# Kernel tuning notes

Measured on AMD Instinct MI355X. Metric: run time of the kernel, lower is better.

## Reference

```python
import jax, jax.numpy as jnp
import numpy as np

L = 8          # n_layer
D = 512        # hidden_size
DIN = 1024     # d_inner = 2*D (Mamba expand=2)
DS = 16        # d_state
DTR = 32       # dt_rank = ceil(D/16)
K = 4          # d_conv
NACT = 3       # n_action_to_predict
ADIM = 4
LOSS_COEF = 1.0

def silu(x):
    return x * jax.nn.sigmoid(x)

def rms(x, w, eps=1e-5):
    return x * jax.lax.rsqrt(jnp.mean(x * x, axis=-1, keepdims=True) + eps) * w

def tokenize(images, states, actions, patch_w, patch_b, state_w, state_b, act_w, act_b):
    # images [b,l,3,224,224] -> 14x14 patches of 3*16*16=768 -> mean-pooled image token
    b, l = images.shape[:2]
    p = images.reshape(b, l, 3, 14, 16, 14, 16).transpose(0, 1, 3, 5, 2, 4, 6).reshape(b, l, 196, 768)
    img = jnp.mean(p @ patch_w.T + patch_b, axis=2)            # [b,l,D] token_type 1
    st = states[:, :, 0] @ state_w.T + state_b                 # [b,l,D] token_type 2
    ac = actions[:, :, :NACT - 1] @ act_w.T + act_b            # [b,l,NACT-1,D] token_type 3
    toks = jnp.concatenate([img[:, :, None], st[:, :, None], ac], axis=2)  # [b,l,1+NACT,D]
    return toks.reshape(b, l * (1 + NACT), D)

def mamba_mixer(x, in_w, cw, cb, xpw, dtw, dtb, alog, dp, ow):
    # x: [b,S,D]
    b, S, _ = x.shape
    xz = x @ in_w.T                                   # [b,S,2*DIN]
    xi, z = xz[..., :DIN], xz[..., DIN:]
    # causal depthwise conv, kernel K
    xp = jnp.pad(xi, ((0, 0), (K - 1, 0), (0, 0)))
    xc = cb + sum(cw[:, k] * xp[:, k:k + S, :] for k in range(K))
    xc = silu(xc)
    proj = xc @ xpw.T                                  # [b,S,DTR+2*DS]
    dtr, Bm, Cm = proj[..., :DTR], proj[..., DTR:DTR + DS], proj[..., DTR + DS:]
    dt = jax.nn.softplus(dtr @ dtw.T + dtb)            # [b,S,DIN]
    A = -jnp.exp(alog)                                 # [DIN,DS]
    dA = jnp.exp(dt[..., None] * A)                    # [b,S,DIN,DS]
    dBx = dt[..., None] * Bm[:, :, None, :] * xc[..., None]
    def step(h, inp):
        a_t, bx_t = inp
        h = a_t * h + bx_t
        return h, h
    _, hs = jax.lax.scan(step, jnp.zeros((b, DIN, DS), x.dtype),
                         (dA.swapaxes(0, 1), dBx.swapaxes(0, 1)))  # hs [S,b,DIN,DS]
    y = jnp.einsum('sbdn,bsn->bsd', hs, Cm) + dp * xc
    return (y * silu(z)) @ ow.T

def _forward(images, seq_length, states, actions, action_labels,
             patch_w, patch_b, state_w, state_b, act_w, act_b,
             norm1_w, in_proj_w, conv_w, conv_b, x_proj_w, dt_w, dt_b,
             A_log, Dp, out_proj_w, norm2_w, fc1_w, fc2_w, norm_f_w,
             head_w, head_b):
    b, l = images.shape[:2]
    hidden = tokenize(images, states, actions, patch_w, patch_b, state_w, state_b, act_w, act_b)
    residual = jnp.zeros_like(hidden)
    for i in range(L):
        residual = hidden + residual
        hidden = mamba_mixer(rms(residual, norm1_w[i]), in_proj_w[i], conv_w[i], conv_b[i],
                             x_proj_w[i], dt_w[i], dt_b[i], A_log[i], Dp[i], out_proj_w[i])
        residual = hidden + residual
        g = rms(residual, norm2_w[i]) @ fc1_w[i].T       # GatedMLP fc1 -> [.., 2*DIN]
        hidden = (g[..., :DIN] * silu(g[..., DIN:])) @ fc2_w[i].T
    residual = hidden + residual
    hidden = rms(residual, norm_f_w)
    # static action-token positions: per-frame tokens [img, state, act, act] -> indices 1..3
    hs = hidden.reshape(b, l, 1 + NACT, D)[:, :, 1:, :]
    action_preds = hs @ head_w.T + head_b                # [b,l,NACT,ADIM]
    mask = (jnp.arange(l)[None, :] < seq_length[:, None]).astype(jnp.float32)
    la = jnp.mean(jnp.abs(action_preds - action_labels), axis=(2, 3))
    la = (la * mask).sum(axis=1) / jnp.clip(mask.sum(axis=1), 1.0)
    loss = jnp.mean(la) * LOSS_COEF
    return loss, action_preds

def setup_inputs() -> dict:
    key = jax.random.key(0)
    ks = iter(jax.random.split(key, 40))
    nrm = lambda shape, s=0.02: s * jax.random.normal(next(ks), shape, dtype=jnp.float32)
    inp = {
        'images': jax.random.normal(next(ks), (2, 64, 3, 224, 224), jnp.float32),
        'seq_length': jax.random.randint(next(ks), (2,), 1, 65),
        'states': jax.random.normal(next(ks), (2, 64, NACT, 7), jnp.float32),
        'actions': jax.random.normal(next(ks), (2, 64, NACT, ADIM), jnp.float32),
        'action_labels': jax.random.normal(next(ks), (2, 64, NACT, ADIM), jnp.float32),
        'patch_w': nrm((D, 768)), 'patch_b': jnp.zeros((D,), jnp.float32),
        'state_w': nrm((D, 7)), 'state_b': jnp.zeros((D,), jnp.float32),
        'act_w': nrm((D, ADIM)), 'act_b': jnp.zeros((D,), jnp.float32),
        'norm1_w': jnp.ones((L, D), jnp.float32),
        'in_proj_w': nrm((L, 2 * DIN, D)),
        'conv_w': nrm((L, DIN, K), 0.1), 'conv_b': jnp.zeros((L, DIN), jnp.float32),
        'x_proj_w': nrm((L, DTR + 2 * DS, DIN)),
        'dt_w': nrm((L, DIN, DTR)), 'dt_b': jnp.full((L, DIN), -4.6, jnp.float32),
        'A_log': jnp.log(jnp.broadcast_to(jnp.arange(1, DS + 1, dtype=jnp.float32), (L, DIN, DS))).copy(),
        'Dp': jnp.ones((L, DIN), jnp.float32),
        'out_proj_w': nrm((L, D, DIN)),
        'norm2_w': jnp.ones((L, D), jnp.float32),
        'fc1_w': nrm((L, 2 * DIN, D)), 'fc2_w': nrm((L, D, DIN)),
        'norm_f_w': jnp.ones((D,), jnp.float32),
        'head_w': nrm((ADIM, D)), 'head_b': jnp.zeros((ADIM,), jnp.float32),
    }
    return inp

def reference(images, seq_length, states, actions, action_labels,
              patch_w, patch_b, state_w, state_b, act_w, act_b,
              norm1_w, in_proj_w, conv_w, conv_b, x_proj_w, dt_w, dt_b,
              A_log, Dp, out_proj_w, norm2_w, fc1_w, fc2_w, norm_f_w,
              head_w, head_b):
    return _forward(images, seq_length, states, actions, action_labels,
                    patch_w, patch_b, state_w, state_b, act_w, act_b,
                    norm1_w, in_proj_w, conv_w, conv_b, x_proj_w, dt_w, dt_b,
                    A_log, Dp, out_proj_w, norm2_w, fc1_w, fc2_w, norm_f_w,
                    head_w, head_b)
```

## Files before the change

### kernel.cpp

```cpp
#include <hip/hip_runtime.h>


#define NTOK 512
#define SEQ  256
#define CS   32

typedef __attribute__((ext_vector_type(8))) short bf16x8;
typedef __attribute__((ext_vector_type(16))) float f32x16;

__device__ __forceinline__ float silu_f(float x) { return x / (1.0f + expf(-x)); }
__device__ __forceinline__ float softplus_f(float x) {
  return (x > 20.0f) ? x : log1pf(expf(x));
}

__device__ __forceinline__ void split_pack(float4 v, uint2* hi, uint2* lo) {
  uint ux = __float_as_uint(v.x), uy = __float_as_uint(v.y);
  uint uz = __float_as_uint(v.z), uw = __float_as_uint(v.w);
  hi->x = (ux >> 16) | (uy & 0xffff0000u);
  hi->y = (uz >> 16) | (uw & 0xffff0000u);
  float lx = v.x - __uint_as_float(ux & 0xffff0000u);
  float ly = v.y - __uint_as_float(uy & 0xffff0000u);
  float lz = v.z - __uint_as_float(uz & 0xffff0000u);
  float lw = v.w - __uint_as_float(uw & 0xffff0000u);
  lo->x = (__float_as_uint(lx) >> 16) | (__float_as_uint(ly) & 0xffff0000u);
  lo->y = (__float_as_uint(lz) >> 16) | (__float_as_uint(lw) & 0xffff0000u);
}

__global__ __launch_bounds__(256) void gemm_bs_k(const float* __restrict__ A,
                                                 const float* __restrict__ B,
                                                 float* __restrict__ C,
                                                 int M, int N, int K, int Kc) {
  __shared__ alignas(16) ushort sAh[2][2][2][512];
  __shared__ alignas(16) ushort sAl[2][2][2][512];
  __shared__ alignas(16) ushort sBh[2][2][2][512];
  __shared__ alignas(16) ushort sBl[2][2][2][512];
  int t = threadIdx.x;
  int bn = blockIdx.x, bm = blockIdx.y, z = blockIdx.z;
  const float* Ab = A + (size_t)bm * 64 * K + (size_t)z * Kc;
  const float* Bb = B + (size_t)bn * 64 * K + (size_t)z * Kc;
  float* Cb = C + (size_t)z * M * N;
  int r = t >> 2, kc = (t & 3) << 2;
  int st = r >> 5, m = r & 31;
  int off = ((kc >> 3) << 8) + (m << 3) + (kc & 7);
  int w = t >> 6, lane = t & 63;
  int wr = w >> 1, wc = w & 1;

  f32x16 acc;
#pragma unroll
  for (int i = 0; i < 16; ++i) acc[i] = 0.f;

  int ns = Kc >> 5;
  const float* Ar = Ab + (size_t)r * K + kc;
  const float* Br = Bb + (size_t)r * K + kc;
  float4 a0 = *(const float4*)&Ar[0];
  float4 a1 = *(const float4*)&Ar[16];
  float4 b0 = *(const float4*)&Br[0];
  float4 b1 = *(const float4*)&Br[16];
  {
    uint2 hi, lo;
    split_pack(a0, &hi, &lo);
    *(uint2*)&sAh[0][0][st][off] = hi; *(uint2*)&sAl[0][0][st][off] = lo;
    split_pack(a1, &hi, &lo);
    *(uint2*)&sAh[0][1][st][off] = hi; *(uint2*)&sAl[0][1][st][off] = lo;
    split_pack(b0, &hi, &lo);
    *(uint2*)&sBh[0][0][st][off] = hi; *(uint2*)&sBl[0][0][st][off] = lo;
    split_pack(b1, &hi, &lo);
    *(uint2*)&sBh[0][1][st][off] = hi; *(uint2*)&sBl[0][1][st][off] = lo;
  }
  __syncthreads();
  for (int ssi = 0; ssi < ns; ++ssi) {
    int buf = ssi & 1;
    if (ssi + 1 < ns) {
      a0 = *(const float4*)&Ar[(ssi + 1) * 32];
      a1 = *(const float4*)&Ar[(ssi + 1) * 32 + 16];
      b0 = *(const float4*)&Br[(ssi + 1) * 32];
      b1 = *(const float4*)&Br[(ssi + 1) * 32 + 16];
    }
    bf16x8 ah = *(bf16x8*)&sAh[buf][0][wr][lane << 3];
    bf16x8 al = *(bf16x8*)&sAl[buf][0][wr][lane << 3];
    bf16x8 bh = *(bf16x8*)&sBh[buf][0][wc][lane << 3];
    bf16x8 bl = *(bf16x8*)&sBl[buf][0][wc][lane << 3];
    acc = __builtin_amdgcn_mfma_f32_32x32x16_bf16(ah, bh, acc, 0, 0, 0);
    acc = __builtin_amdgcn_mfma_f32_32x32x16_bf16(al, bh, acc, 0, 0, 0);
    acc = __builtin_amdgcn_mfma_f32_32x32x16_bf16(ah, bl, acc, 0, 0, 0);
    bf16x8 ah1 = *(bf16x8*)&sAh[buf][1][wr][lane << 3];
    bf16x8 al1 = *(bf16x8*)&sAl[buf][1][wr][lane << 3];
    bf16x8 bh1 = *(bf16x8*)&sBh[buf][1][wc][lane << 3];
    bf16x8 bl1 = *(bf16x8*)&sBl[buf][1][wc][lane << 3];
    acc = __builtin_amdgcn_mfma_f32_32x32x16_bf16(ah1, bh1, acc, 0, 0, 0);
    acc = __builtin_amdgcn_mfma_f32_32x32x16_bf16(al1, bh1, acc, 0, 0, 0);
    acc = __builtin_amdgcn_mfma_f32_32x32x16_bf16(ah1, bl1, acc, 0, 0, 0);
    if (ssi + 1 < ns) {
      uint2 hi, lo;
      split_pack(a0, &hi, &lo);
      *(uint2*)&sAh[buf ^ 1][0][st][off] = hi; *(uint2*)&sAl[buf ^ 1][0][st][off] = lo;
      split_pack(a1, &hi, &lo);
      *(uint2*)&sAh[buf ^ 1][1][st][off] = hi; *(uint2*)&sAl[buf ^ 1][1][st][off] = lo;
      split_pack(b0, &hi, &lo);
      *(uint2*)&sBh[buf ^ 1][0][st][off] = hi; *(uint2*)&sBl[buf ^ 1][0][st][off] = lo;
      split_pack(b1, &hi, &lo);
      *(uint2*)&sBh[buf ^ 1][1][st][off] = hi; *(uint2*)&sBl[buf ^ 1][1][st][off] = lo;
    }
    __syncthreads();
  }
  int col = lane & 31, rq = lane >> 5;
  float* Cw = Cb + (size_t)(bm * 64 + wr * 32) * N + bn * 64 + wc * 32 + col;
#pragma unroll
  for (int rg = 0; rg < 16; ++rg) {
    int row = (rg & 3) + ((rg >> 2) << 3) + (rq << 2);
    Cw[(size_t)row * N] = acc[rg];
  }
}

__global__ __launch_bounds__(256) void gemm_an_k(const float* __restrict__ res,
                                                 const float* __restrict__ nw,
                                                 const float* __restrict__ B,
                                                 float* __restrict__ C, int N) {
  __shared__ alignas(16) ushort sAh[2][2][2][512];
  __shared__ alignas(16) ushort sAl[2][2][2][512];
  __shared__ alignas(16) ushort sBh[2][2][2][512];
  __shared__ alignas(16) ushort sBl[2][2][2][512];
  __shared__ float snw[512];
  int t = threadIdx.x;
  int bn = blockIdx.x, bm = blockIdx.y;
  int r = t >> 2, kc = (t & 3) << 2;
  int row = bm * 64 + r;
  int st = r >> 5, m = r & 31;
  int off = ((kc >> 3) << 8) + (m << 3) + (kc & 7);
  int w = t >> 6, lane = t & 63;
  int wr = w >> 1, wc = w & 1;

  if (t < 128) *(float4*)&snw[t * 4] = *(const float4*)&nw[t * 4];

  const float* rp = res + (size_t)row * 512;
  float ss = 0.f;
#pragma unroll 8
  for (int j = 0; j < 32; ++j) {
    float4 v = *(const float4*)&rp[((t & 3) << 2) + j * 16];
    ss += v.x * v.x + v.y * v.y + v.z * v.z + v.w * v.w;
  }
  ss += __shfl_xor(ss, 1, 64);
  ss += __shfl_xor(ss, 2, 64);
  float scale = rsqrtf(ss * (1.0f / 512.0f) + 1e-5f);
  __syncthreads();

  f32x16 acc;
#pragma unroll
  for (int i = 0; i < 16; ++i) acc[i] = 0.f;

  const float* Ar = rp + kc;
  const float* Br = B + (size_t)(bn * 64 + r) * 512 + kc;
  float4 a0 = *(const float4*)&Ar[0];
  float4 a1 = *(const float4*)&Ar[16];
  float4 b0 = *(const float4*)&Br[0];
  float4 b1 = *(const float4*)&Br[16];
  {
    float4 w0 = *(const float4*)&snw[kc];
    float4 w1 = *(const float4*)&snw[kc + 16];
    float4 p0 = {a0.x * scale * w0.x, a0.y * scale * w0.y,
                 a0.z * scale * w0.z, a0.w * scale * w0.w};
    float4 p1 = {a1.x * scale * w1.x, a1.y * scale * w1.y,
                 a1.z * scale * w1.z, a1.w * scale * w1.w};
    uint2 hi, lo;
    split_pack(p0, &hi, &lo);
    *(uint2*)&sAh[0][0][st][off] = hi; *(uint2*)&sAl[0][0][st][off] = lo;
    split_pack(p1, &hi, &lo);
    *(uint2*)&sAh[0][1][st][off] = hi; *(uint2*)&sAl[0][1][st][off] = lo;
    split_pack(b0, &hi, &lo);
    *(uint2*)&sBh[0][0][st][off] = hi; *(uint2*)&sBl[0][0][st][off] = lo;
    split_pack(b1, &hi, &lo);
    *(uint2*)&sBh[0][1][st][off] = hi; *(uint2*)&sBl[0][1][st][off] = lo;
  }
  __syncthreads();
  for (int ssi = 0; ssi < 16; ++ssi) {
    int buf = ssi & 1;
    if (ssi + 1 < 16) {
      a0 = *(const float4*)&Ar[(ssi + 1) * 32];
      a1 = *(const float4*)&Ar[(ssi + 1) * 32 + 16];
      b0 = *(const float4*)&Br[(ssi + 1) * 32];
      b1 = *(const float4*)&Br[(ssi + 1) * 32 + 16];
    }
    bf16x8 ah = *(bf16x8*)&sAh[buf][0][wr][lane << 3];
    bf16x8 al = *(bf16x8*)&sAl[buf][0][wr][lane << 3];
    bf16x8 bh = *(bf16x8*)&sBh[buf][0][wc][lane << 3];
    bf16x8 bl = *(bf16x8*)&sBl[buf][0][wc][lane << 3];
    acc = __builtin_amdgcn_mfma_f32_32x32x16_bf16(ah, bh, acc, 0, 0, 0);
    acc = __builtin_amdgcn_mfma_f32_32x32x16_bf16(al, bh, acc, 0, 0, 0);
    acc = __builtin_amdgcn_mfma_f32_32x32x16_bf16(ah, bl, acc, 0, 0, 0);
    bf16x8 ah1 = *(bf16x8*)&sAh[buf][1][wr][lane << 3];
    bf16x8 al1 = *(bf16x8*)&sAl[buf][1][wr][lane << 3];
    bf16x8 bh1 = *(bf16x8*)&sBh[buf][1][wc][lane << 3];
    bf16x8 bl1 = *(bf16x8*)&sBl[buf][1][wc][lane << 3];
    acc = __builtin_amdgcn_mfma_f32_32x32x16_bf16(ah1, bh1, acc, 0, 0, 0);
    acc = __builtin_amdgcn_mfma_f32_32x32x16_bf16(al1, bh1, acc, 0, 0, 0);
    acc = __builtin_amdgcn_mfma_f32_32x32x16_bf16(ah1, bl1, acc, 0, 0, 0);
    if (ssi + 1 < 16) {
      int c0 = (ssi + 1) * 32 + kc;
      float4 w0 = *(const float4*)&snw[c0];
      float4 w1 = *(const float4*)&snw[c0 + 16];
      float4 p0 = {a0.x * scale * w0.x, a0.y * scale * w0.y,
                   a0.z * scale * w0.z, a0.w * scale * w0.w};
      float4 p1 = {a1.x * scale * w1.x, a1.y * scale * w1.y,
                   a1.z * scale * w1.z, a1.w * scale * w1.w};
      uint2 hi, lo;
      split_pack(p0, &hi, &lo);
      *(uint2*)&sAh[buf ^ 1][0][st][off] = hi; *(uint2*)&sAl[buf ^ 1][0][st][off] = lo;
      split_pack(p1, &hi, &lo);
      *(uint2*)&sAh[buf ^ 1][1][st][off] = hi; *(uint2*)&sAl[buf ^ 1][1][st][off] = lo;
      split_pack(b0, &hi, &lo);
      *(uint2*)&sBh[buf ^ 1][0][st][off] = hi; *(uint2*)&sBl[buf ^ 1][0][st][off] = lo;
      split_pack(b1, &hi, &lo);
      *(uint2*)&sBh[buf ^ 1][1][st][off] = hi; *(uint2*)&sBl[buf ^ 1][1][st][off] = lo;
    }
    __syncthreads();
  }
  int col = lane & 31, rq = lane >> 5;
  float* Cw = C + (size_t)(bm * 64 + wr * 32) * N + bn * 64 + wc * 32 + col;
#pragma unroll
  for (int rg = 0; rg < 16; ++rg) {
    int row2 = (rg & 3) + ((rg >> 2) << 3) + (rq << 2);
    Cw[(size_t)row2 * N] = acc[rg];
  }
}

__global__ __launch_bounds__(256) void gemm_rmw_k(const float* __restrict__ A,
                                                  const float* __restrict__ B,
                                                  float* __restrict__ resid) {
  __shared__ alignas(16) ushort sAh[2][2][2][512];
  __shared__ alignas(16) ushort sAl[2][2][2][512];
  __shared__ alignas(16) ushort sBh[2][2][2][512];
  __shared__ alignas(16) ushort sBl[2][2][2][512];
  int t = threadIdx.x;
  int bn = blockIdx.x, bm = blockIdx.y, z = blockIdx.z;
  int r = t >> 2, kc = (t & 3) << 2;
  int st = r >> 5, m = r & 31;
  int off = ((kc >> 3) << 8) + (m << 3) + (kc & 7);
  int w = t >> 6, lane = t & 63;
  int wr = w >> 1, wc = w & 1;

  f32x16 acc;
#pragma unroll
  for (int i = 0; i < 16; ++i) acc[i] = 0.f;

  const float* Ar = A + (size_t)(bm * 64 + r) * 1024 + z * 256 + kc;
  const float* Br = B + (size_t)(bn * 64 + r) * 1024 + z * 256 + kc;
  float4 a0 = *(const float4*)&Ar[0];
  float4 a1 = *(const float4*)&Ar[16];
  float4 b0 = *(const float4*)&Br[0];
  float4 b1 = *(const float4*)&Br[16];
  {
    uint2 hi, lo;
    split_pack(a0, &hi, &lo);
    *(uint2*)&sAh[0][0][st][off] = hi; *(uint2*)&sAl[0][0][st][off] = lo;
    split_pack(a1, &hi, &lo);
    *(uint2*)&sAh[0][1][st][off] = hi; *(uint2*)&sAl[0][1][st][off] = lo;
    split_pack(b0, &hi, &lo);
    *(uint2*)&sBh[0][0][st][off] = hi; *(uint2*)&sBl[0][0][st][off] = lo;
    split_pack(b1, &hi, &lo);
    *(uint2*)&sBh[0][1][st][off] = hi; *(uint2*)&sBl[0][1][st][off] = lo;
  }
  __syncthreads();
  for (int ssi = 0; ssi < 8; ++ssi) {
    int buf = ssi & 1;
    if (ssi + 1 < 8) {
      a0 = *(const float4*)&Ar[(ssi + 1) * 32];
      a1 = *(const float4*)&Ar[(ssi + 1) * 32 + 16];
      b0 = *(const float4*)&Br[(ssi + 1) * 32];
      b1 = *(const float4*)&Br[(ssi + 1) * 32 + 16];
    }
    bf16x8 ah = *(bf16x8*)&sAh[buf][0][wr][lane << 3];
    bf16x8 al = *(bf16x8*)&sAl[buf][0][wr][lane << 3];
    bf16x8 bh = *(bf16x8*)&sBh[buf][0][wc][lane << 3];
    bf16x8 bl = *(bf16x8*)&sBl[buf][0][wc][lane << 3];
    acc = __builtin_amdgcn_mfma_f32_32x32x16_bf16(ah, bh, acc, 0, 0, 0);
    acc = __builtin_amdgcn_mfma_f32_32x32x16_bf16(al, bh, acc, 0, 0, 0);
    acc = __builtin_amdgcn_mfma_f32_32x32x16_bf16(ah, bl, acc, 0, 0, 0);
    bf16x8 ah1 = *(bf16x8*)&sAh[buf][1][wr][lane << 3];
    bf16x8 al1 = *(bf16x8*)&sAl[buf][1][wr][lane << 3];
    bf16x8 bh1 = *(bf16x8*)&sBh[buf][1][wc][lane << 3];
    bf16x8 bl1 = *(bf16x8*)&sBl[buf][1][wc][lane << 3];
    acc = __builtin_amdgcn_mfma_f32_32x32x16_bf16(ah1, bh1, acc, 0, 0, 0);
    acc = __builtin_amdgcn_mfma_f32_32x32x16_bf16(al1, bh1, acc, 0, 0, 0);
    acc = __builtin_amdgcn_mfma_f32_32x32x16_bf16(ah1, bl1, acc, 0, 0, 0);
    if (ssi + 1 < 8) {
      uint2 hi, lo;
      split_pack(a0, &hi, &lo);
      *(uint2*)&sAh[buf ^ 1][0][st][off] = hi; *(uint2*)&sAl[buf ^ 1][0][st][off] = lo;
      split_pack(a1, &hi, &lo);
      *(uint2*)&sAh[buf ^ 1][1][st][off] = hi; *(uint2*)&sAl[buf ^ 1][1][st][off] = lo;
      split_pack(b0, &hi, &lo);
      *(uint2*)&sBh[buf ^ 1][0][st][off] = hi; *(uint2*)&sBl[buf ^ 1][0][st][off] = lo;
      split_pack(b1, &hi, &lo);
      *(uint2*)&sBh[buf ^ 1][1][st][off] = hi; *(uint2*)&sBl[buf ^ 1][1][st][off] = lo;
    }
    __syncthreads();
  }
  int col = lane & 31, rq = lane >> 5;
  float* Cw = resid + (size_t)(bm * 64 + wr * 32) * 512 + bn * 64 + wc * 32 + col;
#pragma unroll
  for (int rg = 0; rg < 16; ++rg) {
    int row = (rg & 3) + ((rg >> 2) << 3) + (rq << 2);
    atomicAdd(&Cw[(size_t)row * 512], acc[rg]);
  }
}

__global__ __launch_bounds__(256) void gemm_glu_rmw_k(const float* __restrict__ G,
                                                      const float* __restrict__ B,
                                                      float* __restrict__ resid) {
  __shared__ alignas(16) ushort sAh[2][2][2][512];
  __shared__ alignas(16) ushort sAl[2][2][2][512];
  __shared__ alignas(16) ushort sBh[2][2][2][512];
  __shared__ alignas(16) ushort sBl[2][2][2][512];
  int t = threadIdx.x;
  int bn = blockIdx.x, bm = blockIdx.y, z = blockIdx.z;
  int r = t >> 2, kc = (t & 3) << 2;
  int st = r >> 5, m = r & 31;
  int off = ((kc >> 3) << 8) + (m << 3) + (kc & 7);
  int w = t >> 6, lane = t & 63;
  int wr = w >> 1, wc = w & 1;

  f32x16 acc;
#pragma unroll
  for (int i = 0; i < 16; ++i) acc[i] = 0.f;

  const float* gr = G + (size_t)(bm * 64 + r) * 2048 + z * 256 + kc;
  const float* Br = B + (size_t)(bn * 64 + r) * 1024 + z * 256 + kc;
  float4 ga0 = *(const float4*)&gr[0];
  float4 gz0 = *(const float4*)&gr[1024];
  float4 ga1 = *(const float4*)&gr[16];
  float4 gz1 = *(const float4*)&gr[1040];
  float4 b0 = *(const float4*)&Br[0];
  float4 b1 = *(const float4*)&Br[16];
  {
    float4 a0 = {ga0.x * silu_f(gz0.x), ga0.y * silu_f(gz0.y),
                 ga0.z * silu_f(gz0.z), ga0.w * silu_f(gz0.w)};
    float4 a1 = {ga1.x * silu_f(gz1.x), ga1.y * silu_f(gz1.y),
                 ga1.z * silu_f(gz1.z), ga1.w * silu_f(gz1.w)};
    uint2 hi, lo;
    split_pack(a0, &hi, &lo);
    *(uint2*)&sAh[0][0][st][off] = hi; *(uint2*)&sAl[0][0][st][off] = lo;
    split_pack(a1, &hi, &lo);
    *(uint2*)&sAh[0][1][st][off] = hi; *(uint2*)&sAl[0][1][st][off] = lo;
    split_pack(b0, &hi, &lo);
    *(uint2*)&sBh[0][0][st][off] = hi; *(uint2*)&sBl[0][0][st][off] = lo;
    split_pack(b1, &hi, &lo);
    *(uint2*)&sBh[0][1][st][off] = hi; *(uint2*)&sBl[0][1][st][off] = lo;
  }
  __syncthreads();
  for (int ssi = 0; ssi < 8; ++ssi) {
    int buf = ssi & 1;
    if (ssi + 1 < 8) {
      ga0 = *(const float4*)&gr[(ssi + 1) * 32];
      gz0 = *(const float4*)&gr[1024 + (ssi + 1) * 32];
      ga1 = *(const float4*)&gr[(ssi + 1) * 32 + 16];
      gz1 = *(const float4*)&gr[1040 + (ssi + 1) * 32];
      b0 = *(const float4*)&Br[(ssi + 1) * 32];
      b1 = *(const float4*)&Br[(ssi + 1) * 32 + 16];
    }
    bf16x8 ah = *(bf16x8*)&sAh[buf][0][wr][lane << 3];
    bf16x8 al = *(bf16x8*)&sAl[buf][0][wr][lane << 3];
    bf16x8 bh = *(bf16x8*)&sBh[buf][0][wc][lane << 3];
    bf16x8 bl = *(bf16x8*)&sBl[buf][0][wc][lane << 3];
    acc = __builtin_amdgcn_mfma_f32_32x32x16_bf16(ah, bh, acc, 0, 0, 0);
    acc = __builtin_amdgcn_mfma_f32_32x32x16_bf16(al, bh, acc, 0, 0, 0);
    acc = __builtin_amdgcn_mfma_f32_32x32x16_bf16(ah, bl, acc, 0, 0, 0);
    bf16x8 ah1 = *(bf16x8*)&sAh[buf][1][wr][lane << 3];
    bf16x8 al1 = *(bf16x8*)&sAl[buf][1][wr][lane << 3];
    bf16x8 bh1 = *(bf16x8*)&sBh[buf][1][wc][lane << 3];
    bf16x8 bl1 = *(bf16x8*)&sBl[buf][1][wc][lane << 3];
    acc = __builtin_amdgcn_mfma_f32_32x32x16_bf16(ah1, bh1, acc, 0, 0, 0);
    acc = __builtin_amdgcn_mfma_f32_32x32x16_bf16(al1, bh1, acc, 0, 0, 0);
    acc = __builtin_amdgcn_mfma_f32_32x32x16_bf16(ah1, bl1, acc, 0, 0, 0);
    if (ssi + 1 < 8) {
      float4 a0 = {ga0.x * silu_f(gz0.x), ga0.y * silu_f(gz0.y),
                   ga0.z * silu_f(gz0.z), ga0.w * silu_f(gz0.w)};
      float4 a1 = {ga1.x * silu_f(gz1.x), ga1.y * silu_f(gz1.y),
                   ga1.z * silu_f(gz1.z), ga1.w * silu_f(gz1.w)};
      uint2 hi, lo;
      split_pack(a0, &hi, &lo);
      *(uint2*)&sAh[buf ^ 1][0][st][off] = hi; *(uint2*)&sAl[buf ^ 1][0][st][off] = lo;
      split_pack(a1, &hi, &lo);
      *(uint2*)&sAh[buf ^ 1][1][st][off] = hi; *(uint2*)&sAl[buf ^ 1][1][st][off] = lo;
      split_pack(b0, &hi, &lo);
      *(uint2*)&sBh[buf ^ 1][0][st][off] = hi; *(uint2*)&sBl[buf ^ 1][0][st][off] = lo;
      split_pack(b1, &hi, &lo);
      *(uint2*)&sBh[buf ^ 1][1][st][off] = hi; *(uint2*)&sBl[buf ^ 1][1][st][off] = lo;
    }
    __syncthreads();
  }
  int col = lane & 31, rq = lane >> 5;
  float* Cw = resid + (size_t)(bm * 64 + wr * 32) * 512 + bn * 64 + wc * 32 + col;
#pragma unroll
  for (int rg = 0; rg < 16; ++rg) {
    int row = (rg & 3) + ((rg >> 2) << 3) + (rq << 2);
    atomicAdd(&Cw[(size_t)row * 512], acc[rg]);
  }
}

__global__ void patch_k(const float* __restrict__ img, float* __restrict__ meanp) {
  int bl = blockIdx.x;
  int t = threadIdx.x;
  int c = t >> 6, hi = (t >> 2) & 15, wi4 = t & 3;
  const float* base0 = img + (size_t)bl * 3 * 50176 + (size_t)c * 50176 +
                       (size_t)hi * 224 + wi4 * 4;
  float4 s = {0.f, 0.f, 0.f, 0.f};
  for (int hb = 0; hb < 14; ++hb) {
    const float* base = base0 + (size_t)hb * 16 * 224;
#pragma unroll
    for (int wb = 0; wb < 14; ++wb) {
      float4 v = *(const float4*)&base[wb * 16];
// ... 294 lines not shown

  float* out = (float*)d_out;

  float* ws = (float*)d_ws;
  float* meanp    = ws; ws += 98304;
  float* residual = ws; ws += 262144;
  float* xz       = ws; ws += 1048576;
  float* xc       = ws; ws += 524288;
  float* proj     = ws; ws += 32768;
  float* dtbuf    = ws; ws += 524288;
  float* yz       = ws; ws += 524288;
  float* labs     = ws; ws += 384;
  float* cpart    = ws; ws += 1048576;

  hipLaunchKernelGGL(patch_k, dim3(128), dim3(192), 0, stream, images, meanp);
  hipLaunchKernelGGL(gemm_bs_k, dim3(8, 2, 8), dim3(256), 0, stream,
                     meanp, patch_w, cpart, 128, 512, 768, 96);
  hipLaunchKernelGGL(tokenize_k, dim3(512), dim3(128), 0, stream, cpart, states, actions,
                     patch_b, state_w, state_b, act_w, act_b, residual);

  for (int i = 0; i < 8; ++i) {
    const float* n1 = norm1_w + i * 512;
    const float* ipw = in_proj_w + (size_t)i * 2048 * 512;
    const float* cw = conv_w + (size_t)i * 4096;
    const float* cb = conv_b + (size_t)i * 1024;
    const float* xpw = x_proj_w + (size_t)i * 65536;
    const float* dtw = dt_w + (size_t)i * 32768;
    const float* dtbias = dt_b + (size_t)i * 1024;
    const float* al = A_log + (size_t)i * 16384;
    const float* dpp = Dp + (size_t)i * 1024;
    const float* opw = out_proj_w + (size_t)i * 524288;
    const float* n2 = norm2_w + i * 512;
    const float* f1 = fc1_w + (size_t)i * 1048576;
    const float* f2 = fc2_w + (size_t)i * 524288;

    hipLaunchKernelGGL(gemm_an_k, dim3(32, 8), dim3(256), 0, stream,
                       residual, n1, ipw, xz, 2048);
    hipLaunchKernelGGL(convproj_k, dim3(512), dim3(256), 0, stream,
                       xz, cw, cb, xpw, dtw, dtbias, xc, proj, dtbuf);
    hipLaunchKernelGGL(scan_k, dim3(512), dim3(512), 0, stream,
                       dtbuf, proj, xc, xz, al, dpp, yz);
    hipLaunchKernelGGL(gemm_rmw_k, dim3(8, 8, 4), dim3(256), 0, stream,
                       yz, opw, residual);
    hipLaunchKernelGGL(gemm_an_k, dim3(32, 8), dim3(256), 0, stream,
                       residual, n2, f1, xz, 2048);
    hipLaunchKernelGGL(gemm_glu_rmw_k, dim3(8, 8, 4), dim3(256), 0, stream,
                       xz, f2, residual);
  }

  hipLaunchKernelGGL(head_k, dim3(384), dim3(64), 0, stream, residual, norm_f_w,
                     head_w, head_b, labels, out + 1, labs);
  hipLaunchKernelGGL(loss_k, dim3(1), dim3(128), 0, stream, labs, seq_length, out);
}
```

Before: 1.193 ms.

## Split GEMM K-chunk across two wave groups with LDS reduction

Result: faster. 1.170 ms (-2.0%).

```diff
diff --git a/kernel.cpp b/kernel.cpp
--- a/kernel.cpp
+++ b/kernel.cpp
@@ -26,24 +26,27 @@
   lo->y = (__float_as_uint(lz) >> 16) | (__float_as_uint(lw) & 0xffff0000u);
 }
 
-__global__ __launch_bounds__(256) void gemm_bs_k(const float* __restrict__ A,
-                                                 const float* __restrict__ B,
-                                                 float* __restrict__ C,
-                                                 int M, int N, int K, int Kc) {
+__global__ __launch_bounds__(512, 2) void gemm_bs_k(const float* __restrict__ A,
+                                                    const float* __restrict__ B,
+                                                    float* __restrict__ C,
+                                                    int M, int N, int K, int Kc) {
   __shared__ alignas(16) ushort sAh[2][2][2][512];
   __shared__ alignas(16) ushort sAl[2][2][2][512];
   __shared__ alignas(16) ushort sBh[2][2][2][512];
   __shared__ alignas(16) ushort sBl[2][2][2][512];
+  __shared__ alignas(64) float sRed[4096];
   int t = threadIdx.x;
   int bn = blockIdx.x, bm = blockIdx.y, z = blockIdx.z;
   const float* Ab = A + (size_t)bm * 64 * K + (size_t)z * Kc;
   const float* Bb = B + (size_t)bn * 64 * K + (size_t)z * Kc;
   float* Cb = C + (size_t)z * M * N;
-  int r = t >> 2, kc = (t & 3) << 2;
+  int r = t >> 3, kc = (t & 7) << 2;
+  int kh = kc >> 4, kc16 = kc & 15;
   int st = r >> 5, m = r & 31;
-  int off = ((kc >> 3) << 8) + (m << 3) + (kc & 7);
+  int off = ((kc16 >> 3) << 8) + (m << 3) + (kc16 & 7);
   int w = t >> 6, lane = t & 63;
-  int wr = w >> 1, wc = w & 1;
+  int g = w >> 2, wq = w & 3;
+  int wr = wq >> 1, wc = wq & 1;
 
   f32x16 acc;
 #pragma unroll
@@ -52,95 +55,87 @@
   int ns = Kc >> 5;
   const float* Ar = Ab + (size_t)r * K + kc;
   const float* Br = Bb + (size_t)r * K + kc;
-  float4 a0 = *(const float4*)&Ar[0];
-  float4 a1 = *(const float4*)&Ar[16];
-  float4 b0 = *(const float4*)&Br[0];
-  float4 b1 = *(const float4*)&Br[16];
+  float4 a4 = *(const float4*)&Ar[0];
+  float4 b4 = *(const float4*)&Br[0];
   {
     uint2 hi, lo;
-    split_pack(a0, &hi, &lo);
-    *(uint2*)&sAh[0][0][st][off] = hi; *(uint2*)&sAl[0][0][st][off] = lo;
-    split_pack(a1, &hi, &lo);
-    *(uint2*)&sAh[0][1][st][off] = hi; *(uint2*)&sAl[0][1][st][off] = lo;
-    split_pack(b0, &hi, &lo);
-    *(uint2*)&sBh[0][0][st][off] = hi; *(uint2*)&sBl[0][0][st][off] = lo;
-    split_pack(b1, &hi, &lo);
-    *(uint2*)&sBh[0][1][st][off] = hi; *(uint2*)&sBl[0][1][st][off] = lo;
+    split_pack(a4, &hi, &lo);
+    *(uint2*)&sAh[0][kh][st][off] = hi; *(uint2*)&sAl[0][kh][st][off] = lo;
+    split_pack(b4, &hi, &lo);
+    *(uint2*)&sBh[0][kh][st][off] = hi; *(uint2*)&sBl[0][kh][st][off] = lo;
   }
   __syncthreads();
   for (int ssi = 0; ssi < ns; ++ssi) {
     int buf = ssi & 1;
     if (ssi + 1 < ns) {
-      a0 = *(const float4*)&Ar[(ssi + 1) * 32];
-      a1 = *(const float4*)&Ar[(ssi + 1) * 32 + 16];
-      b0 = *(const float4*)&Br[(ssi + 1) * 32];
-      b1 = *(const float4*)&Br[(ssi + 1) * 32 + 16];
-    }
-    bf16x8 ah = *(bf16x8*)&sAh[buf][0][wr][lane << 3];
-    bf16x8 al = *(bf16x8*)&sAl[buf][0][wr][lane << 3];
-    bf16x8 bh = *(bf16x8*)&sBh[buf][0][wc][lane << 3];
-    bf16x8 bl = *(bf16x8*)&sBl[buf][0][wc][lane << 3];
+      a4 = *(const float4*)&Ar[(ssi + 1) * 32];
+      b4 = *(const float4*)&Br[(ssi + 1) * 32];
+    }
+    bf16x8 ah = *(bf16x8*)&sAh[buf][g][wr][lane << 3];
+    bf16x8 al = *(bf16x8*)&sAl[buf][g][wr][lane << 3];
+    bf16x8 bh = *(bf16x8*)&sBh[buf][g][wc][lane << 3];
+    bf16x8 bl = *(bf16x8*)&sBl[buf][g][wc][lane << 3];
     acc = __builtin_amdgcn_mfma_f32_32x32x16_bf16(ah, bh, acc, 0, 0, 0);
     acc = __builtin_amdgcn_mfma_f32_32x32x16_bf16(al, bh, acc, 0, 0, 0);
     acc = __builtin_amdgcn_mfma_f32_32x32x16_bf16(ah, bl, acc, 0, 0, 0);
-    bf16x8 ah1 = *(bf16x8*)&sAh[buf][1][wr][lane << 3];
-    bf16x8 al1 = *(bf16x8*)&sAl[buf][1][wr][lane << 3];
-    bf16x8 bh1 = *(bf16x8*)&sBh[buf][1][wc][lane << 3];
-    bf16x8 bl1 = *(bf16x8*)&sBl[buf][1][wc][lane << 3];
-    acc = __builtin_amdgcn_mfma_f32_32x32x16_bf16(ah1, bh1, acc, 0, 0, 0);
-    acc = __builtin_amdgcn_mfma_f32_32x32x16_bf16(al1, bh1, acc, 0, 0, 0);
-    acc = __builtin_amdgcn_mfma_f32_32x32x16_bf16(ah1, bl1, acc, 0, 0, 0);
     if (ssi + 1 < ns) {
       uint2 hi, lo;
-      split_pack(a0, &hi, &lo);
-      *(uint2*)&sAh[buf ^ 1][0][st][off] = hi; *(uint2*)&sAl[buf ^ 1][0][st][off] = lo;
-      split_pack(a1, &hi, &lo);
-      *(uint2*)&sAh[buf ^ 1][1][st][off] = hi; *(uint2*)&sAl[buf ^ 1][1][st][off] = lo;
-      split_pack(b0, &hi, &lo);
-      *(uint2*)&sBh[buf ^ 1][0][st][off] = hi; *(uint2*)&sBl[buf ^ 1][0][st][off] = lo;
-      split_pack(b1, &hi, &lo);
-      *(uint2*)&sBh[buf ^ 1][1][st][off] = hi; *(uint2*)&sBl[buf ^ 1][1][st][off] = lo;
+      split_pack(a4, &hi, &lo);
+      *(uint2*)&sAh[buf ^ 1][kh][st][off] = hi; *(uint2*)&sAl[buf ^ 1][kh][st][off] = lo;
+      split_pack(b4, &hi, &lo);
+      *(uint2*)&sBh[buf ^ 1][kh][st][off] = hi; *(uint2*)&sBl[buf ^ 1][kh][st][off] = lo;
     }
     __syncthreads();
   }
-  int col = lane & 31, rq = lane >> 5;
-  float* Cw = Cb + (size_t)(bm * 64 + wr * 32) * N + bn * 64 + wc * 32 + col;
-#pragma unroll
-  for (int rg = 0; rg < 16; ++rg) {
-    int row = (rg & 3) + ((rg >> 2) << 3) + (rq << 2);
-    Cw[(size_t)row * N] = acc[rg];
-  }
-}
-
-__global__ __launch_bounds__(256) void gemm_an_k(const float* __restrict__ res,
-                                                 const float* __restrict__ nw,
-                                                 const float* __restrict__ B,
-                                                 float* __restrict__ C, int N) {
+  if (g == 1) *(f32x16*)&sRed[(wq * 64 + lane) << 4] = acc;
+  __syncthreads();
+  if (g == 0) {
+    f32x16 o = *(f32x16*)&sRed[(wq * 64 + lane) << 4];
+#pragma unroll
+    for (int i = 0; i < 16; ++i) acc[i] += o[i];
+    int col = lane & 31, rq = lane >> 5;
+    float* Cw = Cb + (size_t)(bm * 64 + wr * 32) * N + bn * 64 + wc * 32 + col;
+#pragma unroll
+    for (int rg = 0; rg < 16; ++rg) {
+      int row = (rg & 3) + ((rg >> 2) << 3) + (rq << 2);
+      Cw[(size_t)row * N] = acc[rg];
+    }
+  }
+}
+
+__global__ __launch_bounds__(512, 2) void gemm_an_k(const float* __restrict__ res,
+                                                    const float* __restrict__ nw,
+                                                    const float* __restrict__ B,
+                                                    float* __restrict__ C, int N) {
   __shared__ alignas(16) ushort sAh[2][2][2][512];
   __shared__ alignas(16) ushort sAl[2][2][2][512];
   __shared__ alignas(16) ushort sBh[2][2][2][512];
   __shared__ alignas(16) ushort sBl[2][2][2][512];
+  __shared__ alignas(64) float sRed[4096];
   __shared__ float snw[512];
   int t = threadIdx.x;
   int bn = blockIdx.x, bm = blockIdx.y;
-  int r = t >> 2, kc = (t & 3) << 2;
+  int r = t >> 3, kc = (t & 7) << 2;
   int row = bm * 64 + r;
+  int kh = kc >> 4, kc16 = kc & 15;
   int st = r >> 5, m = r & 31;
-  int off = ((kc >> 3) << 8) + (m << 3) + (kc & 7);
+  int off = ((kc16 >> 3) << 8) + (m << 3) + (kc16 & 7);
   int w = t >> 6, lane = t & 63;
-  int wr = w >> 1, wc = w & 1;
+  int g = w >> 2, wq = w & 3;
+  int wr = wq >> 1, wc = wq & 1;
 
   if (t < 128) *(float4*)&snw[t * 4] = *(const float4*)&nw[t * 4];
 
   const float* rp = res + (size_t)row * 512;
   float ss = 0.f;
 #pragma unroll 8
-  for (int j = 0; j < 32; ++j) {
-    float4 v = *(const float4*)&rp[((t & 3) << 2) + j * 16];
+  for (int j = 0; j < 16; ++j) {
+    float4 v = *(const float4*)&rp[((t & 7) << 2) + j * 32];
     ss += v.x * v.x + v.y * v.y + v.z * v.z + v.w * v.w;
   }
   ss += __shfl_xor(ss, 1, 64);
   ss += __shfl_xor(ss, 2, 64);
+  ss += __shfl_xor(ss, 4, 64);
   float scale = rsqrtf(ss * (1.0f / 512.0f) + 1e-5f);
   __syncthreads();
 
@@ -150,93 +145,79 @@
 
   const float* Ar = rp + kc;
   const float* Br = B + (size_t)(bn * 64 + r) * 512 + kc;
-  float4 a0 = *(const float4*)&Ar[0];
-  float4 a1 = *(const float4*)&Ar[16];
-  float4 b0 = *(const float4*)&Br[0];
-  float4 b1 = *(const float4*)&Br[16];
+  float4 a4 = *(const float4*)&Ar[0];
+  float4 b4 = *(const float4*)&Br[0];
   {
     float4 w0 = *(const float4*)&snw[kc];
-    float4 w1 = *(const float4*)&snw[kc + 16];
-    float4 p0 = {a0.x * scale * w0.x, a0.y * scale * w0.y,
-                 a0.z * scale * w0.z, a0.w * scale * w0.w};
-    float4 p1 = {a1.x * scale * w1.x, a1.y * scale * w1.y,
-                 a1.z * scale * w1.z, a1.w * scale * w1.w};
+    float4 p0 = {a4.x * scale * w0.x, a4.y * scale * w0.y,
+                 a4.z * scale * w0.z, a4.w * scale * w0.w};
     uint2 hi, lo;
     split_pack(p0, &hi, &lo);
-    *(uint2*)&sAh[0][0][st][off] = hi; *(uint2*)&sAl[0][0][st][off] = lo;
-    split_pack(p1, &hi, &lo);
-    *(uint2*)&sAh[0][1][st][off] = hi; *(uint2*)&sAl[0][1][st][off] = lo;
-    split_pack(b0, &hi, &lo);
-    *(uint2*)&sBh[0][0][st][off] = hi; *(uint2*)&sBl[0][0][st][off] = lo;
-    split_pack(b1, &hi, &lo);
-    *(uint2*)&sBh[0][1][st][off] = hi; *(uint2*)&sBl[0][1][st][off] = lo;
-  }
-  __syncthreads();
+    *(uint2*)&sAh[0][kh][st][off] = hi; *(uint2*)&sAl[0][kh][st][off] = lo;
+    split_pack(b4, &hi, &lo);
+    *(uint2*)&sBh[0][kh][st][off] = hi; *(uint2*)&sBl[0][kh][st][off] = lo;
+  }
+  __syncthreads();
+#pragma unroll
   for (int ssi = 0; ssi < 16; ++ssi) {
     int buf = ssi & 1;
     if (ssi + 1 < 16) {
-      a0 = *(const float4*)&Ar[(ssi + 1) * 32];
-      a1 = *(const float4*)&Ar[(ssi + 1) * 32 + 16];
-      b0 = *(const float4*)&Br[(ssi + 1) * 32];
-      b1 = *(const float4*)&Br[(ssi + 1) * 32 + 16];
-    }
-    bf16x8 ah = *(bf16x8*)&sAh[buf][0][wr][lane << 3];
-    bf16x8 al = *(bf16x8*)&sAl[buf][0][wr][lane << 3];
-    bf16x8 bh = *(bf16x8*)&sBh[buf][0][wc][lane << 3];
-    bf16x8 bl = *(bf16x8*)&sBl[buf][0][wc][lane << 3];
+      a4 = *(const float4*)&Ar[(ssi + 1) * 32];
+      b4 = *(const float4*)&Br[(ssi + 1) * 32];
+    }
+    bf16x8 ah = *(bf16x8*)&sAh[buf][g][wr][lane << 3];
+    bf16x8 al = *(bf16x8*)&sAl[buf][g][wr][lane << 3];
+    bf16x8 bh = *(bf16x8*)&sBh[buf][g][wc][lane << 3];
+    bf16x8 bl = *(bf16x8*)&sBl[buf][g][wc][lane << 3];
     acc = __builtin_amdgcn_mfma_f32_32x32x16_bf16(ah, bh, acc, 0, 0, 0);
     acc = __builtin_amdgcn_mfma_f32_32x32x16_bf16(al, bh, acc, 0, 0, 0);
     acc = __builtin_amdgcn_mfma_f32_32x32x16_bf16(ah, bl, acc, 0, 0, 0);
-    bf16x8 ah1 = *(bf16x8*)&sAh[buf][1][wr][lane << 3];
-    bf16x8 al1 = *(bf16x8*)&sAl[buf][1][wr][lane << 3];
-    bf16x8 bh1 = *(bf16x8*)&sBh[buf][1][wc][lane << 3];
-    bf16x8 bl1 = *(bf16x8*)&sBl[buf][1][wc][lane << 3];
-    acc = __builtin_amdgcn_mfma_f32_32x32x16_bf16(ah1, bh1, acc, 0, 0, 0);
-    acc = __builtin_amdgcn_mfma_f32_32x32x16_bf16(al1, bh1, acc, 0, 0, 0);
-    acc = __builtin_amdgcn_mfma_f32_32x32x16_bf16(ah1, bl1, acc, 0, 0, 0);
     if (ssi + 1 < 16) {
       int c0 = (ssi + 1) * 32 + kc;
       float4 w0 = *(const float4*)&snw[c0];
-      float4 w1 = *(const float4*)&snw[c0 + 16];
-      float4 p0 = {a0.x * scale * w0.x, a0.y * scale * w0.y,
-                   a0.z * scale * w0.z, a0.w * scale * w0.w};
-      float4 p1 = {a1.x * scale * w1.x, a1.y * scale * w1.y,
-                   a1.z * scale * w1.z, a1.w * scale * w1.w};
+      float4 p0 = {a4.x * scale * w0.x, a4.y * scale * w0.y,
+                   a4.z * scale * w0.z, a4.w * scale * w0.w};
       uint2 hi, lo;
       split_pack(p0, &hi, &lo);
-      *(uint2*)&sAh[buf ^ 1][0][st][off] = hi; *(uint2*)&sAl[buf ^ 1][0][st][off] = lo;
-      split_pack(p1, &hi, &lo);
-      *(uint2*)&sAh[buf ^ 1][1][st][off] = hi; *(uint2*)&sAl[buf ^ 1][1][st][off] = lo;
-      split_pack(b0, &hi, &lo);
-      *(uint2*)&sBh[buf ^ 1][0][st][off] = hi; *(uint2*)&sBl[buf ^ 1][0][st][off] = lo;
-      split_pack(b1, &hi, &lo);
-      *(uint2*)&sBh[buf ^ 1][1][st][off] = hi; *(uint2*)&sBl[buf ^ 1][1][st][off] = lo;
+      *(uint2*)&sAh[buf ^ 1][kh][st][off] = hi; *(uint2*)&sAl[buf ^ 1][kh][st][off] = lo;
+      split_pack(b4, &hi, &lo);
+      *(uint2*)&sBh[buf ^ 1][kh][st][off] = hi; *(uint2*)&sBl[buf ^ 1][kh][st][off] = lo;
     }
     __syncthreads();
   }
-  int col = lane & 31, rq = lane >> 5;
-  float* Cw = C + (size_t)(bm * 64 + wr * 32) * N + bn * 64 + wc * 32 + col;
-#pragma unroll
-  for (int rg = 0; rg < 16; ++rg) {
-    int row2 = (rg & 3) + ((rg >> 2) << 3) + (rq << 2);
-    Cw[(size_t)row2 * N] = acc[rg];
-  }
-}
-
-__global__ __launch_bounds__(256) void gemm_rmw_k(const float* __restrict__ A,
-                                                  const float* __restrict__ B,
-                                                  float* __restrict__ resid) {
+  if (g == 1) *(f32x16*)&sRed[(wq * 64 + lane) << 4] = acc;
+  __syncthreads();
+  if (g == 0) {
+    f32x16 o = *(f32x16*)&sRed[(wq * 64 + lane) << 4];
+#pragma unroll
+    for (int i = 0; i < 16; ++i) acc[i] += o[i];
+    int col = lane & 31, rq = lane >> 5;
+    float* Cw = C + (size_t)(bm * 64 + wr * 32) * N + bn * 64 + wc * 32 + col;
+#pragma unroll
+    for (int rg = 0; rg < 16; ++rg) {
+      int row2 = (rg & 3) + ((rg >> 2) << 3) + (rq << 2);
+      Cw[(size_t)row2 * N] = acc[rg];
+    }
+  }
+}
+
+__global__ __launch_bounds__(512, 2) void gemm_rmw_k(const float* __restrict__ A,
+                                                     const float* __restrict__ B,
+                                                     float* __restrict__ resid) {
   __shared__ alignas(16) ushort sAh[2][2][2][512];
   __shared__ alignas(16) ushort sAl[2][2][2][512];
   __shared__ alignas(16) ushort sBh[2][2][2][512];
   __shared__ alignas(16) ushort sBl[2][2][2][512];
+  __shared__ alignas(64) float sRed[4096];
   int t = threadIdx.x;
   int bn = blockIdx.x, bm = blockIdx.y, z = blockIdx.z;
-  int r = t >> 2, kc = (t & 3) << 2;
+  int r = t >> 3, kc = (t & 7) << 2;
+  int kh = kc >> 4, kc16 = kc & 15;
   int st = r >> 5, m = r & 31;
-  int off = ((kc >> 3) << 8) + (m << 3) + (kc & 7);
+  int off = ((kc16 >> 3) << 8) + (m << 3) + (kc16 & 7);
   int w = t >> 6, lane = t & 63;
-  int wr = w >> 1, wc = w & 1;
+  int g = w >> 2, wq = w & 3;
+  int wr = wq >> 1, wc = wq & 1;
 
   f32x16 acc;
 #pragma unroll
@@ -244,80 +225,72 @@
 
   const float* Ar = A + (size_t)(bm * 64 + r) * 1024 + z * 256 + kc;
   const float* Br = B + (size_t)(bn * 64 + r) * 1024 + z * 256 + kc;
-  float4 a0 = *(const float4*)&Ar[0];
-  float4 a1 = *(const float4*)&Ar[16];
-  float4 b0 = *(const float4*)&Br[0];
-  float4 b1 = *(const float4*)&Br[16];
+  float4 a4 = *(const float4*)&Ar[0];
+  float4 b4 = *(const float4*)&Br[0];
   {
     uint2 hi, lo;
-    split_pack(a0, &hi, &lo);
-    *(uint2*)&sAh[0][0][st][off] = hi; *(uint2*)&sAl[0][0][st][off] = lo;
-    split_pack(a1, &hi, &lo);
-    *(uint2*)&sAh[0][1][st][off] = hi; *(uint2*)&sAl[0][1][st][off] = lo;
-    split_pack(b0, &hi, &lo);
-    *(uint2*)&sBh[0][0][st][off] = hi; *(uint2*)&sBl[0][0][st][off] = lo;
-    split_pack(b1, &hi, &lo);
-    *(uint2*)&sBh[0][1][st][off] = hi; *(uint2*)&sBl[0][1][st][off] = lo;
-  }
-  __syncthreads();
+    split_pack(a4, &hi, &lo);
+    *(uint2*)&sAh[0][kh][st][off] = hi; *(uint2*)&sAl[0][kh][st][off] = lo;
+    split_pack(b4, &hi, &lo);
+    *(uint2*)&sBh[0][kh][st][off] = hi; *(uint2*)&sBl[0][kh][st][off] = lo;
+  }
+  __syncthreads();
+#pragma unroll
   for (int ssi = 0; ssi < 8; ++ssi) {
     int buf = ssi & 1;
     if (ssi + 1 < 8) {
-      a0 = *(const float4*)&Ar[(ssi + 1) * 32];
-      a1 = *(const float4*)&Ar[(ssi + 1) * 32 + 16];
-      b0 = *(const float4*)&Br[(ssi + 1) * 32];
-      b1 = *(const float4*)&Br[(ssi + 1) * 32 + 16];
-    }
-    bf16x8 ah = *(bf16x8*)&sAh[buf][0][wr][lane << 3];
-    bf16x8 al = *(bf16x8*)&sAl[buf][0][wr][lane << 3];
-    bf16x8 bh = *(bf16x8*)&sBh[buf][0][wc][lane << 3];
-    bf16x8 bl = *(bf16x8*)&sBl[buf][0][wc][lane << 3];
+      a4 = *(const float4*)&Ar[(ssi + 1) * 32];
+      b4 = *(const float4*)&Br[(ssi + 1) * 32];
+    }
+    bf16x8 ah = *(bf16x8*)&sAh[buf][g][wr][lane << 3];
+    bf16x8 al = *(bf16x8*)&sAl[buf][g][wr][lane << 3];
+    bf16x8 bh = *(bf16x8*)&sBh[buf][g][wc][lane << 3];
+    bf16x8 bl = *(bf16x8*)&sBl[buf][g][wc][lane << 3];
     acc = __builtin_amdgcn_mfma_f32_32x32x16_bf16(ah, bh, acc, 0, 0, 0);
     acc = __builtin_amdgcn_mfma_f32_32x32x16_bf16(al, bh, acc, 0, 0, 0);
     acc = __builtin_amdgcn_mfma_f32_32x32x16_bf16(ah, bl, acc, 0, 0, 0);
-    bf16x8 ah1 = *(bf16x8*)&sAh[buf][1][wr][lane << 3];
-    bf16x8 al1 = *(bf16x8*)&sAl[buf][1][wr][lane << 3];
-    bf16x8 bh1 = *(bf16x8*)&sBh[buf][1][wc][lane << 3];
-    bf16x8 bl1 = *(bf16x8*)&sBl[buf][1][wc][lane << 3];
-    acc = __builtin_amdgcn_mfma_f32_32x32x16_bf16(ah1, bh1, acc, 0, 0, 0);
-    acc = __builtin_amdgcn_mfma_f32_32x32x16_bf16(al1, bh1, acc, 0, 0, 0);
-    acc = __builtin_amdgcn_mfma_f32_32x32x16_bf16(ah1, bl1, acc, 0, 0, 0);
     if (ssi + 1 < 8) {
       uint2 hi, lo;
-      split_pack(a0, &hi, &lo);
-      *(uint2*)&sAh[buf ^ 1][0][st][off] = hi; *(uint2*)&sAl[buf ^ 1][0][st][off] = lo;
-      split_pack(a1, &hi, &lo);
-      *(uint2*)&sAh[buf ^ 1][1][st][off] = hi; *(uint2*)&sAl[buf ^ 1][1][st][off] = lo;
-      split_pack(b0, &hi, &lo);
-      *(uint2*)&sBh[buf ^ 1][0][st][off] = hi; *(uint2*)&sBl[buf ^ 1][0][st][off] = lo;
-      split_pack(b1, &hi, &lo);
-      *(uint2*)&sBh[buf ^ 1][1][st][off] = hi; *(uint2*)&sBl[buf ^ 1][1][st][off] = lo;
+      split_pack(a4, &hi, &lo);
+      *(uint2*)&sAh[buf ^ 1][kh][st][off] = hi; *(uint2*)&sAl[buf ^ 1][kh][st][off] = lo;
+      split_pack(b4, &hi, &lo);
+      *(uint2*)&sBh[buf ^ 1][kh][st][off] = hi; *(uint2*)&sBl[buf ^ 1][kh][st][off] = lo;
     }
     __syncthreads();
   }
-  int col = lane & 31, rq = lane >> 5;
-  float* Cw = resid + (size_t)(bm * 64 + wr * 32) * 512 + bn * 64 + wc * 32 + col;
-#pragma unroll
-  for (int rg = 0; rg < 16; ++rg) {
-    int row = (rg & 3) + ((rg >> 2) << 3) + (rq << 2);
-    atomicAdd(&Cw[(size_t)row * 512], acc[rg]);
-  }
-}
-
-__global__ __launch_bounds__(256) void gemm_glu_rmw_k(const float* __restrict__ G,
-                                                      const float* __restrict__ B,
-                                                      float* __restrict__ resid) {
+  if (g == 1) *(f32x16*)&sRed[(wq * 64 + lane) << 4] = acc;
+  __syncthreads();
+  if (g == 0) {
+    f32x16 o = *(f32x16*)&sRed[(wq * 64 + lane) << 4];
+#pragma unroll
+    for (int i = 0; i < 16; ++i) acc[i] += o[i];
+    int col = lane & 31, rq = lane >> 5;
+    float* Cw = resid + (size_t)(bm * 64 + wr * 32) * 512 + bn * 64 + wc * 32 + col;
+#pragma unroll
+    for (int rg = 0; rg < 16; ++rg) {
+      int row = (rg & 3) + ((rg >> 2) << 3) + (rq << 2);
+      atomicAdd(&Cw[(size_t)row * 512], acc[rg]);
+    }
+  }
+}
+
+__global__ __launch_bounds__(512, 2) void gemm_glu_rmw_k(const float* __restrict__ G,
+                                                         const float* __restrict__ B,
+                                                         float* __restrict__ resid) {
   __shared__ alignas(16) ushort sAh[2][2][2][512];
   __shared__ alignas(16) ushort sAl[2][2][2][512];
   __shared__ alignas(16) ushort sBh[2][2][2][512];
   __shared__ alignas(16) ushort sBl[2][2][2][512];
+  __shared__ alignas(64) float sRed[4096];
   int t = threadIdx.x;
   int bn = blockIdx.x, bm = blockIdx.y, z = blockIdx.z;
-  int r = t >> 2, kc = (t & 3) << 2;
+  int r = t >> 3, kc = (t & 7) << 2;
+  int kh = kc >> 4, kc16 = kc & 15;
   int st = r >> 5, m = r & 31;
-  int off = ((kc >> 3) << 8) + (m << 3) + (kc & 7);
+  int off = ((kc16 >> 3) << 8) + (m << 3) + (kc16 & 7);
   int w = t >> 6, lane = t & 63;
-  int wr = w >> 1, wc = w & 1;
+  int g = w >> 2, wq = w & 3;
+  int wr = wq >> 1, wc = wq & 1;
 
   f32x16 acc;
 #pragma unroll
@@ -325,75 +298,58 @@
 
   const float* gr = G + (size_t)(bm * 64 + r) * 2048 + z * 256 + kc;
   const float* Br = B + (size_t)(bn * 64 + r) * 1024 + z * 256 + kc;
-  float4 ga0 = *(const float4*)&gr[0];
-  float4 gz0 = *(const float4*)&gr[1024];
-  float4 ga1 = *(const float4*)&gr[16];
-  float4 gz1 = *(const float4*)&gr[1040];
-  float4 b0 = *(const float4*)&Br[0];
-  float4 b1 = *(const float4*)&Br[16];
+  float4 ga = *(const float4*)&gr[0];
+  float4 gz = *(const float4*)&gr[1024];
+  float4 b4 = *(const float4*)&Br[0];
   {
-    float4 a0 = {ga0.x * silu_f(gz0.x), ga0.y * silu_f(gz0.y),
-                 ga0.z * silu_f(gz0.z), ga0.w * silu_f(gz0.w)};
-    float4 a1 = {ga1.x * silu_f(gz1.x), ga1.y * silu_f(gz1.y),
-                 ga1.z * silu_f(gz1.z), ga1.w * silu_f(gz1.w)};
+    float4 a4 = {ga.x * silu_f(gz.x), ga.y * silu_f(gz.y),
+                 ga.z * silu_f(gz.z), ga.w * silu_f(gz.w)};
     uint2 hi, lo;
-    split_pack(a0, &hi, &lo);
-    *(uint2*)&sAh[0][0][st][off] = hi; *(uint2*)&sAl[0][0][st][off] = lo;
-    split_pack(a1, &hi, &lo);
-    *(uint2*)&sAh[0][1][st][off] = hi; *(uint2*)&sAl[0][1][st][off] = lo;
-    split_pack(b0, &hi, &lo);
-    *(uint2*)&sBh[0][0][st][off] = hi; *(uint2*)&sBl[0][0][st][off] = lo;
-    split_pack(b1, &hi, &lo);
-    *(uint2*)&sBh[0][1][st][off] = hi; *(uint2*)&sBl[0][1][st][off] = lo;
-  }
-  __syncthreads();
+    split_pack(a4, &hi, &lo);
+    *(uint2*)&sAh[0][kh][st][off] = hi; *(uint2*)&sAl[0][kh][st][off] = lo;
+    split_pack(b4, &hi, &lo);
+    *(uint2*)&sBh[0][kh][st][off] = hi; *(uint2*)&sBl[0][kh][st][off] = lo;
+  }
+  __syncthreads();
+#pragma unroll
   for (int ssi = 0; ssi < 8; ++ssi) {
     int buf = ssi & 1;
     if (ssi + 1 < 8) {
-      ga0 = *(const float4*)&gr[(ssi + 1) * 32];
-      gz0 = *(const float4*)&gr[1024 + (ssi + 1) * 32];
-      ga1 = *(const float4*)&gr[(ssi + 1) * 32 + 16];
-      gz1 = *(const float4*)&gr[1040 + (ssi + 1) * 32];
-      b0 = *(const float4*)&Br[(ssi + 1) * 32];
-      b1 = *(const float4*)&Br[(ssi + 1) * 32 + 16];
-    }
-    bf16x8 ah = *(bf16x8*)&sAh[buf][0][wr][lane << 3];
-    bf16x8 al = *(bf16x8*)&sAl[buf][0][wr][lane << 3];
-    bf16x8 bh = *(bf16x8*)&sBh[buf][0][wc][lane << 3];
-    bf16x8 bl = *(bf16x8*)&sBl[buf][0][wc][lane << 3];
+      ga = *(const float4*)&gr[(ssi + 1) * 32];
+      gz = *(const float4*)&gr[1024 + (ssi + 1) * 32];
+      b4 = *(const float4*)&Br[(ssi + 1) * 32];
+    }
+    bf16x8 ah = *(bf16x8*)&sAh[buf][g][wr][lane << 3];
+    bf16x8 al = *(bf16x8*)&sAl[buf][g][wr][lane << 3];
+    bf16x8 bh = *(bf16x8*)&sBh[buf][g][wc][lane << 3];
+    bf16x8 bl = *(bf16x8*)&sBl[buf][g][wc][lane << 3];
     acc = __builtin_amdgcn_mfma_f32_32x32x16_bf16(ah, bh, acc, 0, 0, 0);
     acc = __builtin_amdgcn_mfma_f32_32x32x16_bf16(al, bh, acc, 0, 0, 0);
     acc = __builtin_amdgcn_mfma_f32_32x32x16_bf16(ah, bl, acc, 0, 0, 0);
-    bf16x8 ah1 = *(bf16x8*)&sAh[buf][1][wr][lane << 3];
-    bf16x8 al1 = *(bf16x8*)&sAl[buf][1][wr][lane << 3];
-    bf16x8 bh1 = *(bf16x8*)&sBh[buf][1][wc][lane << 3];
-    bf16x8 bl1 = *(bf16x8*)&sBl[buf][1][wc][lane << 3];
-    acc = __builtin_amdgcn_mfma_f32_32x32x16_bf16(ah1, bh1, acc, 0, 0, 0);
-    acc = __builtin_amdgcn_mfma_f32_32x32x16_bf16(al1, bh1, acc, 0, 0, 0);
-    acc = __builtin_amdgcn_mfma_f32_32x32x16_bf16(ah1, bl1, acc, 0, 0, 0);
     if (ssi + 1 < 8) {
-      float4 a0 = {ga0.x * silu_f(gz0.x), ga0.y * silu_f(gz0.y),
-                   ga0.z * silu_f(gz0.z), ga0.w * silu_f(gz0.w)};
-      float4 a1 = {ga1.x * silu_f(gz1.x), ga1.y * silu_f(gz1.y),
-                   ga1.z * silu_f(gz1.z), ga1.w * silu_f(gz1.w)};
+      float4 a4 = {ga.x * silu_f(gz.x), ga.y * silu_f(gz.y),
+                   ga.z * silu_f(gz.z), ga.w * silu_f(gz.w)};
       uint2 hi, lo;
-      split_pack(a0, &hi, &lo);
-      *(uint2*)&sAh[buf ^ 1][0][st][off] = hi; *(uint2*)&sAl[buf ^ 1][0][st][off] = lo;
-      split_pack(a1, &hi, &lo);
-      *(uint2*)&sAh[buf ^ 1][1][st][off] = hi; *(uint2*)&sAl[buf ^ 1][1][st][off] = lo;
-      split_pack(b0, &hi, &lo);
-      *(uint2*)&sBh[buf ^ 1][0][st][off] = hi; *(uint2*)&sBl[buf ^ 1][0][st][off] = lo;
-      split_pack(b1, &hi, &lo);
-      *(uint2*)&sBh[buf ^ 1][1][st][off] = hi; *(uint2*)&sBl[buf ^ 1][1][st][off] = lo;
+      split_pack(a4, &hi, &lo);
+      *(uint2*)&sAh[buf ^ 1][kh][st][off] = hi; *(uint2*)&sAl[buf ^ 1][kh][st][off] = lo;
+      split_pack(b4, &hi, &lo);
+      *(uint2*)&sBh[buf ^ 1][kh][st][off] = hi; *(uint2*)&sBl[buf ^ 1][kh][st][off] = lo;
     }
     __syncthreads();
   }
-  int col = lane & 31, rq = lane >> 5;
-  float* Cw = resid + (size_t)(bm * 64 + wr * 32) * 512 + bn * 64 + wc * 32 + col;
-#pragma unroll
-  for (int rg = 0; rg < 16; ++rg) {
-    int row = (rg & 3) + ((rg >> 2) << 3) + (rq << 2);
-    atomicAdd(&Cw[(size_t)row * 512], acc[rg]);
+  if (g == 1) *(f32x16*)&sRed[(wq * 64 + lane) << 4] = acc;
+  __syncthreads();
+  if (g == 0) {
+    f32x16 o = *(f32x16*)&sRed[(wq * 64 + lane) << 4];
+#pragma unroll
+    for (int i = 0; i < 16; ++i) acc[i] += o[i];
+    int col = lane & 31, rq = lane >> 5;
+    float* Cw = resid + (size_t)(bm * 64 + wr * 32) * 512 + bn * 64 + wc * 32 + col;
+#pragma unroll
+    for (int rg = 0; rg < 16; ++rg) {
+      int row = (rg & 3) + ((rg >> 2) << 3) + (rq << 2);
+      atomicAdd(&Cw[(size_t)row * 512], acc[rg]);
+    }
   }
 }
 
@@ -718,7 +674,7 @@
   float* cpart    = ws; ws += 1048576;
 
   hipLaunchKernelGGL(patch_k, dim3(128), dim3(192), 0, stream, images, meanp);
-  hipLaunchKernelGGL(gemm_bs_k, dim3(8, 2, 8), dim3(256), 0, stream,
+  hipLaunchKernelGGL(gemm_bs_k, dim3(8, 2, 8), dim3(512), 0, stream,
                      meanp, patch_w, cpart, 128, 512, 768, 96);
   hipLaunchKernelGGL(tokenize_k, dim3(512), dim3(128), 0, stream, cpart, states, actions,
                      patch_b, state_w, state_b, act_w, act_b, residual);
@@ -738,17 +694,17 @@
     const float* f1 = fc1_w + (size_t)i * 1048576;
     const float* f2 = fc2_w + (size_t)i * 524288;
 
-    hipLaunchKernelGGL(gemm_an_k, dim3(32, 8), dim3(256), 0, stream,
+    hipLaunchKernelGGL(gemm_an_k, dim3(32, 8), dim3(512), 0, stream,
                        residual, n1, ipw, xz, 2048);
     hipLaunchKernelGGL(convproj_k, dim3(512), dim3(256), 0, stream,
                        xz, cw, cb, xpw, dtw, dtbias, xc, proj, dtbuf);
     hipLaunchKernelGGL(scan_k, dim3(512), dim3(512), 0, stream,
                        dtbuf, proj, xc, xz, al, dpp, yz);
-    hipLaunchKernelGGL(gemm_rmw_k, dim3(8, 8, 4), dim3(256), 0, stream,
+    hipLaunchKernelGGL(gemm_rmw_k, dim3(8, 8, 4), dim3(512), 0, stream,
                        yz, opw, residual);
-    hipLaunchKernelGGL(gemm_an_k, dim3(32, 8), dim3(256), 0, stream,
+    hipLaunchKernelGGL(gemm_an_k, dim3(32, 8), dim3(512), 0, stream,
                        residual, n2, f1, xz, 2048);
-    hipLaunchKernelGGL(gemm_glu_rmw_k, dim3(8, 8, 4), dim3(256), 0, stream,
+    hipLaunchKernelGGL(gemm_glu_rmw_k, dim3(8, 8, 4), dim3(512), 0, stream,
                        xz, f2, residual);
   }
 
```
